# Kernel tuning notes

Hardware: AMD Instinct MI355X
Metric: run time of the kernel (lower is better)

Reference implementation:

```python
import jax, jax.numpy as jnp
import numpy as np

N_NODES = 50000
N_EDGES = 800000
N_GRAPHS = 256


def setup_inputs() -> dict:
    key = jax.random.key(0)
    ks = jax.random.split(key, 20)
    s = 0.05
    return {
        "x": jax.random.normal(ks[0], (N_NODES, 128), jnp.float32),
        "edge_index": jax.random.randint(ks[1], (2, N_EDGES), 0, N_NODES, jnp.int64),
        "batch_index": jnp.sort(jax.random.randint(ks[2], (N_NODES,), 0, N_GRAPHS, jnp.int64)),
        "mol_features": jax.random.normal(ks[3], (N_GRAPHS, 256), jnp.float32),
        "gcn_W": jax.random.normal(ks[4], (3, 128, 128), jnp.float32) * s,
        "gcn_b": jax.random.normal(ks[5], (3, 128), jnp.float32) * s,
        "gcn_out_W": jax.random.normal(ks[6], (128, 128), jnp.float32) * s,
        "gcn_out_b": jax.random.normal(ks[7], (128,), jnp.float32) * s,
        "mlp_W": jax.random.normal(ks[8], (2, 256, 256), jnp.float32) * s,
        "mlp_b": jax.random.normal(ks[9], (2, 256), jnp.float32) * s,
        "mlp_out_W": jax.random.normal(ks[10], (64, 256), jnp.float32) * s,
        "mlp_out_b": jax.random.normal(ks[11], (64,), jnp.float32) * s,
        "pred_W1": jax.random.normal(ks[12], (256, 192), jnp.float32) * s,
        "pred_b1": jax.random.normal(ks[13], (256,), jnp.float32) * s,
        "pred_W2": jax.random.normal(ks[14], (256, 256), jnp.float32) * s,
        "pred_b2": jax.random.normal(ks[15], (256,), jnp.float32) * s,
        "out_W": jax.random.normal(ks[16], (1, 256), jnp.float32) * s,
        "out_b": jax.random.normal(ks[17], (1,), jnp.float32) * s,
    }


def reference(x, edge_index, batch_index, mol_features,
              gcn_W, gcn_b, gcn_out_W, gcn_out_b,
              mlp_W, mlp_b, mlp_out_W, mlp_out_b,
              pred_W1, pred_b1, pred_W2, pred_b2, out_W, out_b):
    N = x.shape[0]
    E = edge_index.shape[1]
    G = mol_features.shape[0]
    row, col = edge_index[0], edge_index[1]

    # GCN normalization with self-loops (PyG gcn_norm, symmetric):
    # deg[i] = in-degree(i) + 1 (self loop); norm_e = d^-1/2[row] * d^-1/2[col]
    deg = jax.ops.segment_sum(jnp.ones((E,), x.dtype), col, num_segments=N) + 1.0
    dinv = jax.lax.rsqrt(deg)
    enorm = (dinv[row] * dinv[col])[:, None]     # [E,1]
    self_c = (dinv * dinv)[:, None]              # [N,1] self-loop coefficient

    h1 = x
    for i in range(gcn_W.shape[0]):
        h = h1 @ gcn_W[i].T                      # per-node transform [N,128]
        agg = jax.ops.segment_sum(h[row] * enorm, col, num_segments=N)
        h1 = jax.nn.relu(agg + self_c * h + gcn_b[i])
    h1 = h1 @ gcn_out_W.T + gcn_out_b            # final GCN-branch Linear (no relu)

    # global_mean_pool over batch_index -> [G,128]
    sums = jax.ops.segment_sum(h1, batch_index, num_segments=G)
    counts = jax.ops.segment_sum(jnp.ones((N,), x.dtype), batch_index, num_segments=G)
    h1 = sums / jnp.maximum(counts, 1.0)[:, None]

    # MLP branch: relu after every linear (including last)
    h2 = mol_features
    for i in range(mlp_W.shape[0]):
        h2 = jax.nn.relu(h2 @ mlp_W[i].T + mlp_b[i])
    h2 = jax.nn.relu(h2 @ mlp_out_W.T + mlp_out_b)

    h = jnp.concatenate([h1, h2], axis=1)        # [G,192]
    h = jax.nn.relu(h @ pred_W1.T + pred_b1)
    h = jax.nn.relu(h @ pred_W2.T + pred_b2)
    return h @ out_W.T + out_b                   # [G,1]
```

## Files before the change

### kernel.cpp

```cpp
#include <hip/hip_runtime.h>


typedef __attribute__((ext_vector_type(8))) short short8;
typedef __attribute__((ext_vector_type(4))) float f32x4;

#define BKT 64
#define SL 16
#define CAP 192
#define WCAP 2560
#define NBINBLK 2048
#define HROWS 65536

#define HW_MLP0 0
#define HW_MLP1 65536
#define HW_MLO  131072
#define HW_GCNO 147456
#define HW_PW1  163840
#define HW_PW2  212992
#define HW_TOT  278528

__device__ __forceinline__ unsigned short f2bf(float f) {
    union { float f; unsigned u; } c; c.f = f;
    unsigned u = c.u;
    unsigned r = u + 0x7FFFu + ((u >> 16) & 1u);
    return (unsigned short)(r >> 16);
}
__device__ __forceinline__ float bflo(unsigned w) {
    union { unsigned u; float f; } c; c.u = w << 16; return c.f;
}
__device__ __forceinline__ float bfhi(unsigned w) {
    union { unsigned u; float f; } c; c.u = w & 0xFFFF0000u; return c.f;
}

__global__ void k_init(int* cur, float* pool, float* cnt,
                       const float* __restrict__ gcnW, uint4* __restrict__ Wb,
                       const float* __restrict__ mlpW, const float* __restrict__ mloW,
                       const float* __restrict__ gcnoW, const float* __restrict__ pW1,
                       const float* __restrict__ pW2, unsigned short* __restrict__ Wh,
                       int M, int G) {
    int i = blockIdx.x * 256 + threadIdx.x;
    if (i < M * 16) cur[i] = 0;
    if (i < G * 128) pool[i] = 0.f;
    if (i < G) cnt[i] = 0.f;
    if (i < 3 * 2048) {
        int l = i >> 11, rem = i & 2047;
        int o = rem >> 4, c = rem & 15;
        const float4* s = (const float4*)(gcnW + (size_t)l * 16384 + o * 128 + c * 8);
        float4 a = s[0], b = s[1];
        uint4 v;
        v.x = ((unsigned)f2bf(a.y) << 16) | f2bf(a.x);
        v.y = ((unsigned)f2bf(a.w) << 16) | f2bf(a.z);
        v.z = ((unsigned)f2bf(b.y) << 16) | f2bf(b.x);
        v.w = ((unsigned)f2bf(b.w) << 16) | f2bf(b.z);
        Wb[(l << 11) | (o << 4) | (c ^ (o & 15))] = v;
    }
    int j = i - 8192;
    if (j >= 0 && j < (HW_TOT / 8)) {
        int e = j * 8;
        const float* src;
        if (e < HW_MLO)        src = mlpW  + e;
        else if (e < HW_GCNO)  src = mloW  + (e - HW_MLO);
        else if (e < HW_PW1)   src = gcnoW + (e - HW_GCNO);
        else if (e < HW_PW2)   src = pW1   + (e - HW_PW1);
        else                   src = pW2   + (e - HW_PW2);
        float4 a = *(const float4*)src;
        float4 b = *((const float4*)src + 1);
        uint4 v;
        v.x = ((unsigned)f2bf(a.y) << 16) | f2bf(a.x);
        v.y = ((unsigned)f2bf(a.w) << 16) | f2bf(a.z);
        v.z = ((unsigned)f2bf(b.y) << 16) | f2bf(b.x);
        v.w = ((unsigned)f2bf(b.w) << 16) | f2bf(b.z);
        *(uint4*)(Wh + e) = v;
    }
}

__global__ __launch_bounds__(256) void k_bin(const int* __restrict__ row,
                                             const int* __restrict__ col,
                                             int* __restrict__ cur,
                                             unsigned* __restrict__ gbin,
                                             int E, int C) {
    const int x = blockIdx.x & (SL - 1);
    int e0 = blockIdx.x * C, e1 = min(E, e0 + C);
    for (int e = e0 + threadIdx.x; e < e1; e += 256) {
        int c = col[e];
        int cell = (c >> 6) * SL + x;
        int cnt = atomicAdd(&cur[cell << 4], 1);
        gbin[cell * CAP + cnt] = (unsigned)row[e] | ((unsigned)(c & 63) << 16);
    }
}

__global__ __launch_bounds__(256) void k_csr(const unsigned* __restrict__ gbin,
                                             const int* __restrict__ cur,
                                             int* __restrict__ rs,
                                             unsigned short* __restrict__ rd,
                                             float* __restrict__ dinv,
                                             unsigned short* __restrict__ csrf,
                                             const float* __restrict__ x,
                                             unsigned short* __restrict__ xb,
                                             int N) {
    const int b = blockIdx.x, t = threadIdx.x;
    __shared__ int hcnt[64], lcur[64], fills[SL];
    __shared__ float sdinv[64];
    if (t < 64) hcnt[t] = 0;
    if (t < SL) fills[t] = cur[(b * SL + t) << 4];
    __syncthreads();
    #pragma unroll 4
    for (int xx = 0; xx < SL; ++xx) {
        int cbase = (b * SL + xx) * CAP, fill = fills[xx];
        for (int i = t; i < fill; i += 256)
            atomicAdd(&hcnt[(gbin[cbase + i] >> 16) & 63], 1);
    }
    __syncthreads();
    if (t < 64) {
        int v = hcnt[t], xs = v;
        #pragma unroll
        for (int off = 1; off < 64; off <<= 1) {
            int u = __shfl_up(xs, off, 64);
            if (t >= off) xs += u;
        }
        int excl = xs - v;
        lcur[t] = excl;
        float d = rsqrtf((float)v + 1.0f);
        sdinv[t] = d;
        int node = b * 64 + t;
        rs[node] = b * WCAP + excl;
        rd[node] = (unsigned short)v;
        dinv[node] = d;
    }
    __syncthreads();
    #pragma unroll 4
    for (int xx = 0; xx < SL; ++xx) {
        int cbase = (b * SL + xx) * CAP, fill = fills[xx];
        for (int i = t; i < fill; i += 256) {
            unsigned v = gbin[cbase + i];
            int p = atomicAdd(&lcur[(v >> 16) & 63], 1);
            csrf[b * WCAP + p] = (unsigned short)(v & 0xFFFFu);
        }
    }
    const int node0 = b * 64;
    #pragma unroll
    for (int it = 0; it < 4; ++it) {
        int i = t + it * 256;
        int nd = node0 + (i >> 4);
        if (nd < N) {
            int ch = i & 15;
            float d = sdinv[i >> 4];
            const float4* s = (const float4*)(x + (size_t)nd * 128 + ch * 8);
            float4 a = s[0], bb = s[1];
            uint4 o;
            o.x = ((unsigned)f2bf(d * a.y) << 16) | f2bf(d * a.x);
            o.y = ((unsigned)f2bf(d * a.w) << 16) | f2bf(d * a.z);
            o.z = ((unsigned)f2bf(d * bb.y) << 16) | f2bf(d * bb.x);
            o.w = ((unsigned)f2bf(d * bb.w) << 16) | f2bf(d * bb.z);
            *(uint4*)(xb + (size_t)nd * 128 + ch * 8) = o;
        }
    }
}

__global__ __launch_bounds__(256) void k_agg(const unsigned short* __restrict__ h,
                                             unsigned short* __restrict__ y,
                                             const float* __restrict__ dinv,
                                             const int* __restrict__ rs,
                                             const unsigned short* __restrict__ rd,
                                             const unsigned short* __restrict__ csrf,
                                             int N) {
    const int lane = threadIdx.x & 63;
    const int n = blockIdx.x * 4 + (threadIdx.x >> 6);
    if (n >= N) return;
    const int fg = lane & 15;
    const int slot = lane >> 4;
    const int s = rs[n], e = s + rd[n];

    float acc[8] = {0.f, 0.f, 0.f, 0.f, 0.f, 0.f, 0.f, 0.f};
    for (int base = s; base < e; base += 16) {
        int src_l = csrf[base + fg];
        #pragma unroll
        for (int i = 0; i < 4; ++i) {
            int j = i * 4 + slot;
            bool ok = (base + j) < e;
            int src = __shfl(src_l, j, 16);
            src = ok ? src : 0;
            uint4 v = *(const uint4*)(h + (size_t)src * 128 + fg * 8);
            v.x = ok ? v.x : 0u; v.y = ok ? v.y : 0u;
            v.z = ok ? v.z : 0u; v.w = ok ? v.w : 0u;
            acc[0] += bflo(v.x); acc[1] += bfhi(v.x);
            acc[2] += bflo(v.y); acc[3] += bfhi(v.y);
            acc[4] += bflo(v.z); acc[5] += bfhi(v.z);
            acc[6] += bflo(v.w); acc[7] += bfhi(v.w);
        }
    }
    #pragma unroll
    for (int r = 0; r < 8; ++r) {
        acc[r] += __shfl_xor(acc[r], 16, 64);
        acc[r] += __shfl_xor(acc[r], 32, 64);
    }
    if (slot == 0) {
        float dn = dinv[n];
        uint4 hv = *(const uint4*)(h + (size_t)n * 128 + fg * 8);
        float sv[8] = {bflo(hv.x), bfhi(hv.x), bflo(hv.y), bfhi(hv.y),
                       bflo(hv.z), bfhi(hv.z), bflo(hv.w), bfhi(hv.w)};
        unsigned short ob[8];
        #pragma unroll
        for (int r = 0; r < 8; ++r) ob[r] = f2bf(dn * (acc[r] + sv[r]));
        uint4 o;
        o.x = ((unsigned)ob[1] << 16) | ob[0];
        o.y = ((unsigned)ob[3] << 16) | ob[2];
        o.z = ((unsigned)ob[5] << 16) | ob[4];
        o.w = ((unsigned)ob[7] << 16) | ob[6];
        *(uint4*)(y + (size_t)n * 128 + fg * 8) = o;
    }
}

__global__ __launch_bounds__(256) void k_mm(const unsigned short* __restrict__ A,
                                            const uint4* __restrict__ Wb,
                                            const float* __restrict__ bias,
                                            const float* __restrict__ dscale,
                                            unsigned short* __restrict__ C, int N) {
    __shared__ uint4 Wsh[2048];
    const int tid = threadIdx.x;
    #pragma unroll
    for (int it = 0; it < 8; ++it)
        Wsh[tid + it * 256] = Wb[tid + it * 256];

    const int lane = tid & 63;
    const int wv = tid >> 6;
    const int l15 = lane & 15, quad = lane >> 4;
    const int arow_i = blockIdx.x * 64 + wv * 16 + l15;
    const unsigned short* arow = A + (size_t)min(arow_i, N - 1) * 128;

    f32x4 acc[8];
    #pragma unroll
    for (int ct = 0; ct < 8; ++ct) acc[ct] = (f32x4){0.f, 0.f, 0.f, 0.f};

    __syncthreads();
    #pragma unroll
    for (int kiter = 0; kiter < 4; ++kiter) {
        short8 af = *(const short8*)(arow + kiter * 32 + quad * 8);
        const int cswz = (kiter * 4 + quad) ^ l15;
        #pragma unroll
        for (int ct = 0; ct < 8; ++ct) {
            short8 bf = *(const short8*)(&Wsh[((ct * 16 + l15) << 4) | cswz]);
            acc[ct] = __builtin_amdgcn_mfma_f32_16x16x32_bf16(af, bf, acc[ct], 0, 0, 0);
        }
    }

    const int rbase = blockIdx.x * 64 + wv * 16 + quad * 4;
    float ds[4];
    #pragma unroll
    for (int r = 0; r < 4; ++r) {
        int rr = rbase + r;
        ds[r] = (dscale && rr < N) ? dscale[rr] : 1.f;
    }
    #pragma unroll
    for (int ct = 0; ct < 8; ++ct) {
        int colc = ct * 16 + l15;
        float bcol = bias[colc];
        #pragma unroll
        for (int r = 0; r < 4; ++r) {
            int rr = rbase + r;
            if (rr < N) {
                float v = fmaxf(acc[ct][r] + bcol, 0.f) * ds[r];
                C[(size_t)rr * 128 + colc] = f2bf(v);
            }
        }
    }
}

__global__ __launch_bounds__(256) void k_pool(const unsigned short* __restrict__ h,
                                              const int* __restrict__ batch,
                                              float* __restrict__ pool,
                                              float* __restrict__ cnt, int N) {
    int t = threadIdx.x;
    int fg = t & 15, sg = t >> 4;
    int n0 = blockIdx.x * 512 + sg * 32;
    if (n0 >= N) return;
    int n1 = min(n0 + 32, N);
    int gprev = batch[n0];
    float racc[8] = {0.f, 0.f, 0.f, 0.f, 0.f, 0.f, 0.f, 0.f};
    float rcnt = 0.f;
    for (int n = n0; n < n1; ++n) {
        int g = batch[n];
        if (g != gprev) {
            float* dst = pool + (size_t)gprev * 128 + fg * 8;
            #pragma unroll
            for (int r = 0; r < 8; ++r) atomicAdd(dst + r, racc[r]);
            if (fg == 0) atomicAdd(&cnt[gprev], rcnt);
            #pragma unroll
            for (int r = 0; r < 8; ++r) racc[r] = 0.f;
            rcnt = 0.f; gprev = g;
        }
        uint4 v = *(const uint4*)(h + (size_t)n * 128 + fg * 8);
        racc[0] += bflo(v.x); racc[1] += bfhi(v.x);
        racc[2] += bflo(v.y); racc[3] += bfhi(v.y);
        racc[4] += bflo(v.z); racc[5] += bfhi(v.z);
        racc[6] += bflo(v.w); racc[7] += bfhi(v.w);
        rcnt += 1.f;
    }
    float* dst = pool + (size_t)gprev * 128 + fg * 8;
    #pragma unroll
    for (int r = 0; r < 8; ++r) atomicAdd(dst + r, racc[r]);
    if (fg == 0) atomicAdd(&cnt[gprev], rcnt);
}

__global__ __launch_bounds__(256) void k_head(
    const unsigned short* __restrict__ Wh,
    const float* __restrict__ pool, const float* __restrict__ cnt,
    const float* __restrict__ mol,
    const float* __restrict__ mlpb, const float* __restrict__ mlob,
    const float* __restrict__ gcnob,
    const float* __restrict__ pb1, const float* __restrict__ pb2,
    const float* __restrict__ oW, const float* __restrict__ ob,
    float* __restrict__ out, int G) {
    const int g0 = blockIdx.x * 16;
    const int t = threadIdx.x;
    const int lane = t & 63, wv = t >> 6;
    const int l15 = lane & 15, quad = lane >> 4;
    __shared__ unsigned short A[16][264], B[16][264], Cc[16][200], Mn[16][136];
    __shared__ float red[4][16];

    for (int i = t; i < 16 * 256; i += 256) {
        int g = i >> 8, k = i & 255;
        A[g][k] = f2bf(mol[(size_t)(g0 + g) * 256 + k]);
    }
    for (int i = t; i < 16 * 128; i += 256) {
        int g = i >> 7, k = i & 127;
        float c = cnt[g0 + g];
        Mn[g][k] = f2bf(pool[(size_t)(g0 + g) * 128 + k] / fmaxf(c, 1.f));
    }
    __syncthreads();

    auto do_tile = [&](const unsigned short* actb, int astr, int K,
                       const unsigned short* W, int orow,
                       const float* __restrict__ bias, int bidx,
                       unsigned short* dstb, int dstr, int ocol, bool dorelu) {
        f32x4 c = {0.f, 0.f, 0.f, 0.f};
        for (int kt = 0; kt < (K >> 5); ++kt) {
            short8 af = *(const short8*)(actb + (size_t)l15 * astr + kt * 32 + quad * 8);
            short8 bf = *(const short8*)(W + (size_t)orow * K + kt * 32 + quad * 8);
            c = __builtin_amdgcn_mfma_f32_16x16x32_bf16(af, bf, c, 0, 0, 0);
        }
        float bb = bias[bidx];
        #pragma unroll
        for (int r = 0; r < 4; ++r) {
            int g = quad * 4 + r;
            float v = c[r] + bb;
            if (dorelu) v = fmaxf(v, 0.f);
            dstb[(size_t)g * dstr + ocol] = f2bf(v);
        }
    };

    #pragma unroll
    for (int nt = 0; nt < 4; ++nt) {
        int o = (wv * 4 + nt) * 16 + l15;
        do_tile(&A[0][0], 264, 256, Wh + HW_MLP0, o, mlpb, o, &B[0][0], 264, o, true);
    }
    __syncthreads();
    #pragma unroll
    for (int nt = 0; nt < 4; ++nt) {
        int o = (wv * 4 + nt) * 16 + l15;
        do_tile(&B[0][0], 264, 256, Wh + HW_MLP1, o, mlpb + 256, o, &A[0][0], 264, o, true);
    }
    __syncthreads();
    #pragma unroll
    for (int j = 0; j < 3; ++j) {
        int tile = wv * 3 + j;
        if (tile < 8) {
            int o = tile * 16 + l15;
            do_tile(&Mn[0][0], 136, 128, Wh + HW_GCNO, o, gcnob, o, &Cc[0][0], 200, o, false);
        } else {
            int om = (tile - 8) * 16 + l15;
            do_tile(&A[0][0], 264, 256, Wh + HW_MLO, om, mlob, om, &Cc[0][0], 200, 128 + om, true);
        }
    }
    __syncthreads();
    #pragma unroll
    for (int nt = 0; nt < 4; ++nt) {
        int o = (wv * 4 + nt) * 16 + l15;
        do_tile(&Cc[0][0], 200, 192, Wh + HW_PW1, o, pb1, o, &B[0][0], 264, o, true);
    }
    __syncthreads();
    {
        float pacc[4] = {0.f, 0.f, 0.f, 0.f};
        #pragma unroll
        for (int nt = 0; nt < 4; ++nt) {
            int o = (wv * 4 + nt) * 16 + l15;
            f32x4 c = {0.f, 0.f, 0.f, 0.f};
            #pragma unroll
            for (int kt = 0; kt < 8; ++kt) {
                short8 af = *(const short8*)(&B[0][0] + (size_t)l15 * 264 + kt * 32 + quad * 8);
                short8 bf = *(const short8*)(Wh + HW_PW2 + (size_t)o * 256 + kt * 32 + quad * 8);
                c = __builtin_amdgcn_mfma_f32_16x16x32_bf16(af, bf, c, 0, 0, 0);
            }
            float bb = pb2[o], wo = oW[o];
            #pragma unroll
            for (int r = 0; r < 4; ++r)
                pacc[r] += fmaxf(c[r] + bb, 0.f) * wo;
        }
        #pragma unroll
        for (int off = 1; off < 16; off <<= 1)
            #pragma unroll
            for (int r = 0; r < 4; ++r)
                pacc[r] += __shfl_xor(pacc[r], off, 64);
        if (l15 == 0) {
            #pragma unroll
            for (int r = 0; r < 4; ++r)
                red[wv][quad * 4 + r] = pacc[r];
        }
    }
    __syncthreads();
    if (t < 16) {
        float s = red[0][t] + red[1][t] + red[2][t] + red[3][t] + ob[0];
        if (g0 + t < G) out[g0 + t] = s;
    }
}

extern "C" void kernel_launch(void* const* d_in, const int* in_sizes, int n_in,
                              void* d_out, int out_size, void* d_ws, size_t ws_size,
                              hipStream_t stream) {
    const float* x     = (const float*)d_in[0];
    const int*   ei    = (const int*)d_in[1];
    const int*   batch = (const int*)d_in[2];
    const float* mol   = (const float*)d_in[3];
    const float* gcnW  = (const float*)d_in[4];
    const float* gcnb  = (const float*)d_in[5];
    const float* gcnoW = (const float*)d_in[6];
    const float* gcnob = (const float*)d_in[7];
    const float* mlpW  = (const float*)d_in[8];
    const float* mlpb  = (const float*)d_in[9];
    const float* mloW  = (const float*)d_in[10];
    const float* mlob  = (const float*)d_in[11];
    const float* pW1   = (const float*)d_in[12];
    const float* pb1   = (const float*)d_in[13];
    const float* pW2   = (const float*)d_in[14];
    const float* pb2   = (const float*)d_in[15];
    const float* oW    = (const float*)d_in[16];
    const float* ob    = (const float*)d_in[17];

    const int N = in_sizes[0] / 128;
    const int E = in_sizes[1] / 2;
    const int G = in_sizes[3] / 256;
    const int* row = ei;
    const int* col = ei + E;

    const int NBK = (N + BKT - 1) / BKT;
    const int M = NBK * SL;
    const int C = (E + NBINBLK - 1) / NBINBLK;

    char* p = (char*)d_ws;
    auto alloc = [&](size_t bytes) {
        char* q = p;
        p += (bytes + 255) & ~(size_t)255;
        return (void*)q;
    };
    int*    rs    = (int*)alloc((size_t)NBK * 64 * 4);
    unsigned short* rd = (unsigned short*)alloc((size_t)NBK * 64 * 2);
    float*  dinv  = (float*)alloc((size_t)NBK * 64 * 4);
    int*    cur   = (int*)alloc((size_t)M * 16 * 4);
    unsigned* gbin = (unsigned*)alloc((size_t)M * CAP * 4);
    unsigned short* csrf = (unsigned short*)alloc(((size_t)NBK * WCAP + 32) * 2);
    unsigned short* xb   = (unsigned short*)alloc((size_t)HROWS * 128 * 2);
    unsigned short* bufA = (unsigned short*)alloc((size_t)HROWS * 128 * 2);
    unsigned short* bufB = (unsigned short*)alloc((size_t)HROWS * 128 * 2);
    uint4*  Wb    = (uint4*)alloc((size_t)3 * 2048 * 16);
    unsigned short* Wh = (unsigned short*)alloc((size_t)HW_TOT * 2);
    float*  pool  = (float*)alloc((size_t)G * 128 * 4);
    float*  cnt   = (float*)alloc((size_t)G * 4);

    const int initblocks = (M * 16 + 255) / 256;

    k_init<<<initblocks, 256, 0, stream>>>(cur, pool, cnt, gcnW, Wb,
                                           mlpW, mloW, gcnoW, pW1, pW2, Wh, M, G);
    k_bin<<<NBINBLK, 256, 0, stream>>>(row, col, cur, gbin, E, C);
    k_csr<<<NBK, 256, 0, stream>>>(gbin, cur, rs, rd, dinv, csrf, x, xb, N);

    const int mmblocks = (N + 63) / 64;
    const int aggblocks = (N + 3) / 4;
    const unsigned short* src = xb;
    for (int l = 0; l < 3; ++l) {
        k_agg<<<aggblocks, 256, 0, stream>>>(src, bufA, dinv, rs, rd, csrf, N);
        k_mm<<<mmblocks, 256, 0, stream>>>(bufA, Wb + (size_t)l * 2048,
                                           gcnb + (size_t)l * 128,
                                           (l < 2) ? dinv : (const float*)nullptr,
                                           bufB, N);
        src = bufB;
    }
    k_pool<<<(N + 511) / 512, 256, 0, stream>>>(bufB, batch, pool, cnt, N);
    k_head<<<(G + 15) / 16, 256, 0, stream>>>(
        Wh, pool, cnt, mol, mlpb, mlob, gcnob, pb1, pb2, oW, ob,
        (float*)d_out, G);
}
```

Before: 348.5 us.

## Fuse GCN aggregation and MFMA matmul into one kernel per layer

Merges the per-layer gather-aggregate kernel and the bf16 MFMA transform into a single 1024-thread kernel. Each block aggregates 64 nodes into an LDS tile, then 16 waves multiply it by the weights held in LDS, each wave covering a 16x32 output tile. This removes the global round-trip of the aggregated buffer and three kernel launches. In exchange, each block loads a 32KB weight tile for only 64 rows, and the large block with a sync barrier between the irregular gather and the MFMA phase may lower occupancy and overlap.

New measurement: 338.2 us. -3.0%, faster.

```diff
diff --git a/kernel.cpp b/kernel.cpp
--- a/kernel.cpp
+++ b/kernel.cpp
@@ -157,94 +157,96 @@
     }
 }
 
-__global__ __launch_bounds__(256) void k_agg(const unsigned short* __restrict__ h,
-                                             unsigned short* __restrict__ y,
-                                             const float* __restrict__ dinv,
-                                             const int* __restrict__ rs,
-                                             const unsigned short* __restrict__ rd,
-                                             const unsigned short* __restrict__ csrf,
-                                             int N) {
-    const int lane = threadIdx.x & 63;
-    const int n = blockIdx.x * 4 + (threadIdx.x >> 6);
-    if (n >= N) return;
+__global__ __launch_bounds__(1024, 8) void k_fused(
+    const unsigned short* __restrict__ h,
+    const uint4* __restrict__ Wb,
+    const float* __restrict__ bias,
+    const float* __restrict__ dscale,
+    const float* __restrict__ dinv,
+    const int* __restrict__ rs,
+    const unsigned short* __restrict__ rd,
+    const unsigned short* __restrict__ csrf,
+    unsigned short* __restrict__ C, int N) {
+    __shared__ uint4 Wsh[2048];
+    __shared__ unsigned short Ash[64][136];
+
+    const int t = threadIdx.x;
+    Wsh[t] = Wb[t];
+    Wsh[t + 1024] = Wb[t + 1024];
+
+    const int lane = t & 63;
+    const int wv = t >> 6;
     const int fg = lane & 15;
     const int slot = lane >> 4;
-    const int s = rs[n], e = s + rd[n];
-
-    float acc[8] = {0.f, 0.f, 0.f, 0.f, 0.f, 0.f, 0.f, 0.f};
-    for (int base = s; base < e; base += 16) {
-        int src_l = csrf[base + fg];
-        #pragma unroll
-        for (int i = 0; i < 4; ++i) {
-            int j = i * 4 + slot;
-            bool ok = (base + j) < e;
-            int src = __shfl(src_l, j, 16);
-            src = ok ? src : 0;
-            uint4 v = *(const uint4*)(h + (size_t)src * 128 + fg * 8);
-            v.x = ok ? v.x : 0u; v.y = ok ? v.y : 0u;
-            v.z = ok ? v.z : 0u; v.w = ok ? v.w : 0u;
-            acc[0] += bflo(v.x); acc[1] += bfhi(v.x);
-            acc[2] += bflo(v.y); acc[3] += bfhi(v.y);
-            acc[4] += bflo(v.z); acc[5] += bfhi(v.z);
-            acc[6] += bflo(v.w); acc[7] += bfhi(v.w);
-        }
-    }
-    #pragma unroll
-    for (int r = 0; r < 8; ++r) {
-        acc[r] += __shfl_xor(acc[r], 16, 64);
-        acc[r] += __shfl_xor(acc[r], 32, 64);
-    }
-    if (slot == 0) {
-        float dn = dinv[n];
-        uint4 hv = *(const uint4*)(h + (size_t)n * 128 + fg * 8);
-        float sv[8] = {bflo(hv.x), bfhi(hv.x), bflo(hv.y), bfhi(hv.y),
-                       bflo(hv.z), bfhi(hv.z), bflo(hv.w), bfhi(hv.w)};
-        unsigned short ob[8];
-        #pragma unroll
-        for (int r = 0; r < 8; ++r) ob[r] = f2bf(dn * (acc[r] + sv[r]));
-        uint4 o;
-        o.x = ((unsigned)ob[1] << 16) | ob[0];
-        o.y = ((unsigned)ob[3] << 16) | ob[2];
-        o.z = ((unsigned)ob[5] << 16) | ob[4];
-        o.w = ((unsigned)ob[7] << 16) | ob[6];
-        *(uint4*)(y + (size_t)n * 128 + fg * 8) = o;
-    }
-}
-
-__global__ __launch_bounds__(256) void k_mm(const unsigned short* __restrict__ A,
-                                            const uint4* __restrict__ Wb,
-                                            const float* __restrict__ bias,
-                                            const float* __restrict__ dscale,
-                                            unsigned short* __restrict__ C, int N) {
-    __shared__ uint4 Wsh[2048];
-    const int tid = threadIdx.x;
-    #pragma unroll
-    for (int it = 0; it < 8; ++it)
-        Wsh[tid + it * 256] = Wb[tid + it * 256];
-
-    const int lane = tid & 63;
-    const int wv = tid >> 6;
-    const int l15 = lane & 15, quad = lane >> 4;
-    const int arow_i = blockIdx.x * 64 + wv * 16 + l15;
-    const unsigned short* arow = A + (size_t)min(arow_i, N - 1) * 128;
-
-    f32x4 acc[8];
-    #pragma unroll
-    for (int ct = 0; ct < 8; ++ct) acc[ct] = (f32x4){0.f, 0.f, 0.f, 0.f};
-
-    __syncthreads();
+
+    for (int s = 0; s < 4; ++s) {
+        const int lrow = wv * 4 + s;
+        const int n = blockIdx.x * 64 + lrow;
+        if (n < N) {
+            const int st = rs[n], e = st + rd[n];
+            float acc[8] = {0.f, 0.f, 0.f, 0.f, 0.f, 0.f, 0.f, 0.f};
+            for (int base = st; base < e; base += 16) {
+                int src_l = csrf[base + fg];
+                #pragma unroll
+                for (int i = 0; i < 4; ++i) {
+                    int j = i * 4 + slot;
+                    bool ok = (base + j) < e;
+                    int src = __shfl(src_l, j, 16);
+                    src = ok ? src : 0;
+                    uint4 v = *(const uint4*)(h + (size_t)src * 128 + fg * 8);
+                    v.x = ok ? v.x : 0u; v.y = ok ? v.y : 0u;
+                    v.z = ok ? v.z : 0u; v.w = ok ? v.w : 0u;
+                    acc[0] += bflo(v.x); acc[1] += bfhi(v.x);
+                    acc[2] += bflo(v.y); acc[3] += bfhi(v.y);
+                    acc[4] += bflo(v.z); acc[5] += bfhi(v.z);
+                    acc[6] += bflo(v.w); acc[7] += bfhi(v.w);
+                }
+            }
+            #pragma unroll
+            for (int r = 0; r < 8; ++r) {
+                acc[r] += __shfl_xor(acc[r], 16, 64);
+                acc[r] += __shfl_xor(acc[r], 32, 64);
+            }
+            if (slot == 0) {
+                float dn = dinv[n];
+                uint4 hv = *(const uint4*)(h + (size_t)n * 128 + fg * 8);
+                float sv[8] = {bflo(hv.x), bfhi(hv.x), bflo(hv.y), bfhi(hv.y),
+                               bflo(hv.z), bfhi(hv.z), bflo(hv.w), bfhi(hv.w)};
+                unsigned short ob[8];
+                #pragma unroll
+                for (int r = 0; r < 8; ++r) ob[r] = f2bf(dn * (acc[r] + sv[r]));
+                uint4 o;
+                o.x = ((unsigned)ob[1] << 16) | ob[0];
+                o.y = ((unsigned)ob[3] << 16) | ob[2];
+                o.z = ((unsigned)ob[5] << 16) | ob[4];
+                o.w = ((unsigned)ob[7] << 16) | ob[6];
+                *(uint4*)(&Ash[lrow][fg * 8]) = o;
+            }
+        } else if (slot == 0) {
+            uint4 z = {0u, 0u, 0u, 0u};
+            *(uint4*)(&Ash[lrow][fg * 8]) = z;
+        }
+    }
+    __syncthreads();
+
+    const int rt = wv & 3, cp = wv >> 2;
+    const int l15 = fg, quad = slot;
+    f32x4 acc2[2];
+    acc2[0] = (f32x4){0.f, 0.f, 0.f, 0.f};
+    acc2[1] = (f32x4){0.f, 0.f, 0.f, 0.f};
     #pragma unroll
     for (int kiter = 0; kiter < 4; ++kiter) {
-        short8 af = *(const short8*)(arow + kiter * 32 + quad * 8);
+        short8 af = *(const short8*)(&Ash[rt * 16 + l15][kiter * 32 + quad * 8]);
         const int cswz = (kiter * 4 + quad) ^ l15;
         #pragma unroll
-        for (int ct = 0; ct < 8; ++ct) {
+        for (int cc = 0; cc < 2; ++cc) {
+            int ct = cp * 2 + cc;
             short8 bf = *(const short8*)(&Wsh[((ct * 16 + l15) << 4) | cswz]);
-            acc[ct] = __builtin_amdgcn_mfma_f32_16x16x32_bf16(af, bf, acc[ct], 0, 0, 0);
-        }
-    }
-
-    const int rbase = blockIdx.x * 64 + wv * 16 + quad * 4;
+            acc2[cc] = __builtin_amdgcn_mfma_f32_16x16x32_bf16(af, bf, acc2[cc], 0, 0, 0);
+        }
+    }
+
+    const int rbase = blockIdx.x * 64 + rt * 16 + quad * 4;
     float ds[4];
     #pragma unroll
     for (int r = 0; r < 4; ++r) {
@@ -252,14 +254,14 @@
         ds[r] = (dscale && rr < N) ? dscale[rr] : 1.f;
     }
     #pragma unroll
-    for (int ct = 0; ct < 8; ++ct) {
-        int colc = ct * 16 + l15;
+    for (int cc = 0; cc < 2; ++cc) {
+        int colc = (cp * 2 + cc) * 16 + l15;
         float bcol = bias[colc];
         #pragma unroll
         for (int r = 0; r < 4; ++r) {
             int rr = rbase + r;
             if (rr < N) {
-                float v = fmaxf(acc[ct][r] + bcol, 0.f) * ds[r];
+                float v = fmaxf(acc2[cc][r] + bcol, 0.f) * ds[r];
                 C[(size_t)rr * 128 + colc] = f2bf(v);
             }
         }
@@ -473,18 +475,17 @@
     k_bin<<<NBINBLK, 256, 0, stream>>>(row, col, cur, gbin, E, C);
     k_csr<<<NBK, 256, 0, stream>>>(gbin, cur, rs, rd, dinv, csrf, x, xb, N);
 
-    const int mmblocks = (N + 63) / 64;
-    const int aggblocks = (N + 3) / 4;
+    const int fblocks = (N + 63) / 64;
+    unsigned short* dst[3] = {bufA, bufB, bufA};
     const unsigned short* src = xb;
     for (int l = 0; l < 3; ++l) {
-        k_agg<<<aggblocks, 256, 0, stream>>>(src, bufA, dinv, rs, rd, csrf, N);
-        k_mm<<<mmblocks, 256, 0, stream>>>(bufA, Wb + (size_t)l * 2048,
-                                           gcnb + (size_t)l * 128,
-                                           (l < 2) ? dinv : (const float*)nullptr,
-                                           bufB, N);
-        src = bufB;
-    }
-    k_pool<<<(N + 511) / 512, 256, 0, stream>>>(bufB, batch, pool, cnt, N);
+        k_fused<<<fblocks, 1024, 0, stream>>>(src, Wb + (size_t)l * 2048,
+                                              gcnb + (size_t)l * 128,
+                                              (l < 2) ? dinv : (const float*)nullptr,
+                                              dinv, rs, rd, csrf, dst[l], N);
+        src = dst[l];
+    }
+    k_pool<<<(N + 511) / 512, 256, 0, stream>>>(bufA, batch, pool, cnt, N);
     k_head<<<(G + 15) / 16, 256, 0, stream>>>(
         Wh, pool, cnt, mol, mlpb, mlob, gcnob, pb1, pb2, oW, ob,
         (float*)d_out, G);
```
